# Performance work log

Measured on AMD Instinct MI355X. Metric: run time of the kernel, lower is better.

The kernel has to match this reference:

```python
import jax, jax.numpy as jnp
import numpy as np


def _iir_forward(b_coeff, rho, psi, u_in, y_init, u_init):
    # Coefficient computation: stable 2nd-order resonator parameterization
    r = jax.nn.sigmoid(rho)
    theta = jnp.pi * jax.nn.sigmoid(psi)
    a1 = -2.0 * r * jnp.cos(theta)
    a2 = r * r

    B, T = u_in.shape
    nb = b_coeff.shape[0]  # number of FIR taps (n_b)

    # FIR (moving-average) part, fully vectorized over batch and time:
    # v[t] = sum_k b[k] * u[t-k]; past inputs come from u_init = [u[-1], u[-2], ...]
    u_ext = jnp.concatenate([u_init[:, ::-1], u_in], axis=1)  # [B, T + nb - 1], time-ordered
    v = jnp.zeros_like(u_in)
    for k in range(nb):  # small fixed loop over filter taps
        v = v + b_coeff[k] * jax.lax.dynamic_slice_in_dim(u_ext, nb - 1 - k, T, axis=1)

    # AR (recursive) part: y[t] = v[t] - a1*y[t-1] - a2*y[t-2]  (sequential scan over time)
    def step(carry, v_t):
        y1, y2 = carry  # y[t-1], y[t-2], each [B]
        y = v_t - a1 * y1 - a2 * y2
        return (y, y1), y

    init = (y_init[:, 0], y_init[:, 1])  # [y[-1], y[-2]] per lfiltic convention
    _, y = jax.lax.scan(step, init, v.T)  # y: [T, B]
    return y.T  # [B, T]


def setup_inputs() -> dict:
    key = jax.random.key(0)
    k1, k2, k3, k4 = jax.random.split(key, 4)
    B, T, NB = 1024, 16384, 3
    return {
        "b_coeff": 0.1 * jax.random.normal(k1, (NB,), dtype=jnp.float32),
        "rho": jnp.asarray(jax.random.normal(k2, (), dtype=jnp.float32) + 0.9),
        "psi": jnp.asarray(jax.random.normal(k3, (), dtype=jnp.float32) * 0.5),
        "u_in": jax.random.normal(k4, (B, T), dtype=jnp.float32),
        "y_init": jnp.zeros((B, 2), dtype=jnp.float32),
        "u_init": jnp.zeros((B, NB - 1), dtype=jnp.float32),
    }


def reference(b_coeff, rho, psi, u_in, y_init, u_init):
    return _iir_forward(b_coeff, rho, psi, u_in, y_init, u_init)
```

## Files before the change

### kernel.cpp

```cpp
#include <hip/hip_runtime.h>
#include <math.h>


#define TLEN  16384
#define HALF  8192
#define NT    256
#define CK    32
#define NCH   256
#define CARRY_OFF (2*NCH)
#define LDS_FLOATS (2*NCH + 2)

__device__ __forceinline__ void mat2_sq(float& m00, float& m01, float& m10, float& m11) {
    float t00 = m00*m00 + m01*m10;
    float t01 = m00*m01 + m01*m11;
    float t10 = m10*m00 + m11*m10;
    float t11 = m10*m01 + m11*m11;
    m00 = t00; m01 = t01; m10 = t10; m11 = t11;
}

__device__ __forceinline__ void bar_lgkm() {
    asm volatile("s_waitcnt lgkmcnt(0)" ::: "memory");
    __builtin_amdgcn_s_barrier();
    __builtin_amdgcn_sched_barrier(0);
}

__global__ __launch_bounds__(NT, 4)
void iir_kernel(const float* __restrict__ bc,
                const float* __restrict__ rho_p,
                const float* __restrict__ psi_p,
                const float* __restrict__ u_in,
                const float* __restrict__ y_init,
                const float* __restrict__ u_init,
                float* __restrict__ y_out)
{
    __shared__ float lds[LDS_FLOATS];
    const int row = blockIdx.x;
    const int tid = threadIdx.x;

    const float* urow = u_in  + (size_t)row * TLEN;
    float*       orow = y_out + (size_t)row * TLEN;

    float4 uv[8];
    {
        const float4* up = (const float4*)(urow + CK * tid);
        #pragma unroll
        for (int j = 0; j < 8; ++j) uv[j] = up[j];
    }
    float hm2, hm1;
    if (tid == 0) {
        hm2 = u_init[2*row + 1];
        hm1 = u_init[2*row + 0];
    } else {
        float2 hh = *(const float2*)(urow + CK*tid - 2);
        hm2 = hh.x; hm1 = hh.y;
    }

    const float rho = rho_p[0];
    const float psi = psi_p[0];
    const float r   = 1.0f / (1.0f + expf(-rho));
    const float th  = 3.14159265358979323846f / (1.0f + expf(-psi));
    const float a1  = -2.0f * r * cosf(th);
    const float a2  = r * r;
    const float b0  = bc[0], b1 = bc[1], b2 = bc[2];

    float v[CK];

    #pragma unroll
    for (int h = 0; h < 2; ++h) {
        float um2 = hm2, um1 = hm1;
        float y1 = 0.0f, y2 = 0.0f;
        #define STEP(UC, IDX) {                                        \
            float uc_ = (UC);                                          \
            float vv_ = fmaf(b2, um2, fmaf(b1, um1, b0 * uc_));        \
            v[IDX] = vv_;                                              \
            float y_ = fmaf(-a1, y1, fmaf(-a2, y2, vv_));              \
            y2 = y1; y1 = y_;                                          \
            um2 = um1; um1 = uc_; }
        #pragma unroll
        for (int q = 0; q < 8; ++q) {
            float4 u4 = uv[q];
            STEP(u4.x, 4*q + 0);
            STEP(u4.y, 4*q + 1);
            STEP(u4.z, 4*q + 2);
            STEP(u4.w, 4*q + 3);
        }
        #undef STEP

        *(float2*)&lds[2*tid] = make_float2(y1, y2);

        if (h == 0) {
            const float4* up = (const float4*)(urow + HALF + CK * tid);
            #pragma unroll
            for (int j = 0; j < 8; ++j) uv[j] = up[j];
            float2 hh = *(const float2*)(urow + HALF + CK*tid - 2);
            hm2 = hh.x; hm1 = hh.y;
        }

        bar_lgkm();

        if (tid < 64) {
            const int l = tid;
            float m00 = -a1, m01 = -a2, m10 = 1.0f, m11 = 0.0f;
            #pragma unroll
            for (int s = 0; s < 5; ++s) mat2_sq(m00, m01, m10, m11);

            float4 q0 = *(const float4*)&lds[8*l];
            float4 q1 = *(const float4*)&lds[8*l + 4];
            float da[4] = {q0.x, q0.z, q1.x, q1.z};
            float db[4] = {q0.y, q0.w, q1.y, q1.w};

            float seed0 = 0.0f, seed1 = 0.0f;
            if (l == 0) {
                if (h == 0) { seed0 = y_init[2*row]; seed1 = y_init[2*row + 1]; }
                else        { seed0 = lds[CARRY_OFF]; seed1 = lds[CARRY_OFF + 1]; }
            }
            float s0 = seed0, s1 = seed1;
            #pragma unroll
            for (int m = 0; m < 4; ++m) {
                float n0 = fmaf(m00, s0, fmaf(m01, s1, da[m]));
                float n1 = fmaf(m10, s0, fmaf(m11, s1, db[m]));
                s0 = n0; s1 = n1;
            }
            float w00 = m00, w01 = m01, w10 = m10, w11 = m11;
            mat2_sq(w00, w01, w10, w11);
            mat2_sq(w00, w01, w10, w11);
            #pragma unroll
            for (int p = 0; p < 6; ++p) {
                float o0 = __shfl_up(s0, 1 << p);
                float o1 = __shfl_up(s1, 1 << p);
                if (l >= (1 << p)) {
                    s0 = fmaf(w00, o0, fmaf(w01, o1, s0));
                    s1 = fmaf(w10, o0, fmaf(w11, o1, s1));
                }
                if (p < 5) mat2_sq(w00, w01, w10, w11);
            }
            float p0 = __shfl_up(s0, 1);
            float p1 = __shfl_up(s1, 1);
            if (l == 0) { p0 = seed0; p1 = seed1; }
            float c0 = p0, c1 = p1;
            #pragma unroll
            for (int m = 0; m < 4; ++m) {
                *(float2*)&lds[2*(4*l + m)] = make_float2(c0, c1);
                float n0 = fmaf(m00, c0, fmaf(m01, c1, da[m]));
                float n1 = fmaf(m10, c0, fmaf(m11, c1, db[m]));
                c0 = n0; c1 = n1;
            }
            if (l == 63 && h == 0) {
                lds[CARRY_OFF]     = c0;
                lds[CARRY_OFF + 1] = c1;
            }
        }
        bar_lgkm();

        float2 inc = *(const float2*)&lds[2*tid];
        float y1f = inc.x, y2f = inc.y;
        float* oh = orow + h * HALF + CK * tid;
        #pragma unroll
        for (int q = 0; q < 8; ++q) {
            float ya = fmaf(-a1, y1f, fmaf(-a2, y2f, v[4*q + 0]));
            float yb = fmaf(-a1, ya,  fmaf(-a2, y1f, v[4*q + 1]));
            float yc = fmaf(-a1, yb,  fmaf(-a2, ya,  v[4*q + 2]));
            float yd = fmaf(-a1, yc,  fmaf(-a2, yb,  v[4*q + 3]));
            float4 w; w.x = ya; w.y = yb; w.z = yc; w.w = yd;
            *(float4*)(oh + 4*q) = w;
            y2f = yc; y1f = yd;
        }
        if (h == 0) bar_lgkm();
    }
}

extern "C" void kernel_launch(void* const* d_in, const int* in_sizes, int n_in,
                              void* d_out, int out_size, void* d_ws, size_t ws_size,
                              hipStream_t stream) {
    const float* bc    = (const float*)d_in[0];
    const float* rho   = (const float*)d_in[1];
    const float* psi   = (const float*)d_in[2];
    const float* u_in  = (const float*)d_in[3];
    const float* y_in  = (const float*)d_in[4];
    const float* u_ini = (const float*)d_in[5];
    float* y = (float*)d_out;
    const int B = in_sizes[3] / TLEN;
    iir_kernel<<<B, NT, 0, stream>>>(bc, rho, psi, u_in, y_in, u_ini, y);
}
```

Measured before the change: 132.1 us.

## Stage input and output through swizzled LDS for coalesced global access

```diff
diff --git a/kernel.cpp b/kernel.cpp
--- a/kernel.cpp
+++ b/kernel.cpp
@@ -7,8 +7,11 @@
 #define NT    256
 #define CK    32
 #define NCH   256
-#define CARRY_OFF (2*NCH)
-#define LDS_FLOATS (2*NCH + 2)
+#define SCAN_OFF  HALF
+#define CARRY_OFF (SCAN_OFF + 2*NCH)
+#define LDS_FLOATS (CARRY_OFF + 2)
+
+__device__ __forceinline__ int swz(int s) { return s ^ ((s >> 3) & 7); }
 
 __device__ __forceinline__ void mat2_sq(float& m00, float& m01, float& m10, float& m11) {
     float t00 = m00*m00 + m01*m10;
@@ -34,18 +37,17 @@
                 float* __restrict__ y_out)
 {
     __shared__ float lds[LDS_FLOATS];
+    float4* lds4 = (float4*)lds;
     const int row = blockIdx.x;
     const int tid = threadIdx.x;
 
     const float* urow = u_in  + (size_t)row * TLEN;
     float*       orow = y_out + (size_t)row * TLEN;
+    const float4* up  = (const float4*)urow;
 
     float4 uv[8];
-    {
-        const float4* up = (const float4*)(urow + CK * tid);
-        #pragma unroll
-        for (int j = 0; j < 8; ++j) uv[j] = up[j];
-    }
+    #pragma unroll
+    for (int k = 0; k < 8; ++k) uv[k] = up[tid + k * NT];
     float hm2, hm1;
     if (tid == 0) {
         hm2 = u_init[2*row + 1];
@@ -63,10 +65,22 @@
     const float a2  = r * r;
     const float b0  = bc[0], b1 = bc[1], b2 = bc[2];
 
+    const int xr = tid & 7;
     float v[CK];
 
     #pragma unroll
     for (int h = 0; h < 2; ++h) {
+        #pragma unroll
+        for (int k = 0; k < 8; ++k) {
+            int g = tid + k * NT;
+            lds4[swz(g)] = uv[k];
+        }
+        bar_lgkm();
+
+        float4 u4[8];
+        #pragma unroll
+        for (int j = 0; j < 8; ++j) u4[j] = lds4[8*tid + (j ^ xr)];
+
         float um2 = hm2, um1 = hm1;
         float y1 = 0.0f, y2 = 0.0f;
         #define STEP(UC, IDX) {                                        \
@@ -78,20 +92,18 @@
             um2 = um1; um1 = uc_; }
         #pragma unroll
         for (int q = 0; q < 8; ++q) {
-            float4 u4 = uv[q];
-            STEP(u4.x, 4*q + 0);
-            STEP(u4.y, 4*q + 1);
-            STEP(u4.z, 4*q + 2);
-            STEP(u4.w, 4*q + 3);
+            STEP(u4[q].x, 4*q + 0);
+            STEP(u4[q].y, 4*q + 1);
+            STEP(u4[q].z, 4*q + 2);
+            STEP(u4[q].w, 4*q + 3);
         }
         #undef STEP
 
-        *(float2*)&lds[2*tid] = make_float2(y1, y2);
+        *(float2*)&lds[SCAN_OFF + 2*tid] = make_float2(y1, y2);
 
         if (h == 0) {
-            const float4* up = (const float4*)(urow + HALF + CK * tid);
-            #pragma unroll
-            for (int j = 0; j < 8; ++j) uv[j] = up[j];
+            #pragma unroll
+            for (int k = 0; k < 8; ++k) uv[k] = up[(HALF/4) + tid + k * NT];
             float2 hh = *(const float2*)(urow + HALF + CK*tid - 2);
             hm2 = hh.x; hm1 = hh.y;
         }
@@ -104,8 +116,8 @@
             #pragma unroll
             for (int s = 0; s < 5; ++s) mat2_sq(m00, m01, m10, m11);
 
-            float4 q0 = *(const float4*)&lds[8*l];
-            float4 q1 = *(const float4*)&lds[8*l + 4];
+            float4 q0 = *(const float4*)&lds[SCAN_OFF + 8*l];
+            float4 q1 = *(const float4*)&lds[SCAN_OFF + 8*l + 4];
             float da[4] = {q0.x, q0.z, q1.x, q1.z};
             float db[4] = {q0.y, q0.w, q1.y, q1.w};
 
@@ -140,7 +152,7 @@
             float c0 = p0, c1 = p1;
             #pragma unroll
             for (int m = 0; m < 4; ++m) {
-                *(float2*)&lds[2*(4*l + m)] = make_float2(c0, c1);
+                *(float2*)&lds[SCAN_OFF + 2*(4*l + m)] = make_float2(c0, c1);
                 float n0 = fmaf(m00, c0, fmaf(m01, c1, da[m]));
                 float n1 = fmaf(m10, c0, fmaf(m11, c1, db[m]));
                 c0 = n0; c1 = n1;
@@ -152,9 +164,8 @@
         }
         bar_lgkm();
 
-        float2 inc = *(const float2*)&lds[2*tid];
+        float2 inc = *(const float2*)&lds[SCAN_OFF + 2*tid];
         float y1f = inc.x, y2f = inc.y;
-        float* oh = orow + h * HALF + CK * tid;
         #pragma unroll
         for (int q = 0; q < 8; ++q) {
             float ya = fmaf(-a1, y1f, fmaf(-a2, y2f, v[4*q + 0]));
@@ -162,8 +173,16 @@
             float yc = fmaf(-a1, yb,  fmaf(-a2, ya,  v[4*q + 2]));
             float yd = fmaf(-a1, yc,  fmaf(-a2, yb,  v[4*q + 3]));
             float4 w; w.x = ya; w.y = yb; w.z = yc; w.w = yd;
-            *(float4*)(oh + 4*q) = w;
+            lds4[8*tid + (q ^ xr)] = w;
             y2f = yc; y1f = yd;
+        }
+        bar_lgkm();
+
+        float4* op = (float4*)(orow + h * HALF);
+        #pragma unroll
+        for (int k = 0; k < 8; ++k) {
+            int g = tid + k * NT;
+            op[g] = lds4[swz(g)];
         }
         if (h == 0) bar_lgkm();
     }
```

Result: slower. 143.9 us (+8.9%).
